# Kernel tuning notes

Measured on AMD Instinct MI355X. Metric: run time of the kernel, lower is better.

The kernel has to match this reference:

```python
import jax, jax.numpy as jnp
import numpy as np

B, S, DIM = 2, 2048, 1024
N_HEAD, HEAD_DIM = 16, 64


def setup_inputs() -> dict:
    key = jax.random.key(0)
    k1, k2, k3, k4 = jax.random.split(key, 4)
    x = jax.random.normal(k1, (B, S, DIM), dtype=jnp.float32)
    # rotary table: cos/sin pairs, shape [S, head_dim//2, 2]
    half = HEAD_DIM // 2
    inv_freq = 1.0 / (10000.0 ** (jnp.arange(0, half, dtype=jnp.float32) / half))
    t = jnp.arange(S, dtype=jnp.float32)
    ang = t[:, None] * inv_freq[None, :]
    freqs_cis = jnp.stack([jnp.cos(ang), jnp.sin(ang)], axis=-1)  # [S, half, 2]
    # causal boolean mask [1,1,S,S] (True = attend)
    mask = jnp.tril(jnp.ones((S, S), dtype=bool))[None, None]
    wqkv = jax.random.normal(k2, (3 * DIM, DIM), dtype=jnp.float32) * (DIM ** -0.5)
    wo = jax.random.normal(k3, (DIM, DIM), dtype=jnp.float32) * (DIM ** -0.5)
    return {"x": x, "freqs_cis": freqs_cis, "mask": mask, "wqkv": wqkv, "wo": wo}


def apply_rotary_emb(x, freqs_cis):
    # x: [B, S, H, D]; freqs_cis: [S, D//2, 2]
    xs = x.reshape(*x.shape[:-1], -1, 2)  # [B,S,H,D//2,2]
    fc = freqs_cis[None, :, None, :, :]  # [1,S,1,D//2,2]
    xr, xi = xs[..., 0], xs[..., 1]
    cr, ci = fc[..., 0], fc[..., 1]
    out = jnp.stack([xr * cr - xi * ci, xi * cr + xr * ci], axis=-1)
    return out.reshape(x.shape)


def reference(x, freqs_cis, mask, wqkv, wo):
    bsz, seqlen, _ = x.shape
    qkv = jnp.einsum('bsd,ed->bse', x, wqkv)  # [B,S,3*dim]
    q, k, v = jnp.split(qkv, 3, axis=-1)
    q = q.reshape(bsz, seqlen, N_HEAD, HEAD_DIM)
    k = k.reshape(bsz, seqlen, N_HEAD, HEAD_DIM)
    v = v.reshape(bsz, seqlen, N_HEAD, HEAD_DIM)
    q = apply_rotary_emb(q, freqs_cis)
    k = apply_rotary_emb(k, freqs_cis)
    scale = HEAD_DIM ** -0.5
    scores = jnp.einsum('bqhd,bkhd->bhqk', q, k) * scale  # [B,H,S,S]
    scores = jnp.where(mask, scores, jnp.finfo(scores.dtype).min)
    attn = jax.nn.softmax(scores, axis=-1)
    y = jnp.einsum('bhqk,bkhd->bqhd', attn, v).reshape(bsz, seqlen, N_HEAD * HEAD_DIM)
    return jnp.einsum('bse,de->bsd', y, wo)
```

## Files before the change

kernel.cpp:

```cpp
#include <hip/hip_runtime.h>
#include <hip/hip_bf16.h>
#include <stdint.h>


typedef __attribute__((ext_vector_type(8))) __bf16 bf16x8;
typedef __attribute__((ext_vector_type(4))) float f32x4;

union B8 { uint4 u; bf16x8 v; unsigned short us[8]; };

static __device__ __forceinline__ float bf2f(unsigned short u) {
  union { unsigned int ui; float f; } x; x.ui = ((unsigned int)u) << 16; return x.f;
}
static __device__ __forceinline__ unsigned short f2bf(float f) {
  union { float f; unsigned int ui; } x; x.f = f;
  unsigned int r = x.ui + 0x7fffu + ((x.ui >> 16) & 1u);
  return (unsigned short)(r >> 16);
}
static __device__ __forceinline__ f32x4 mfma16(bf16x8 a, bf16x8 b, f32x4 c) {
  return __builtin_amdgcn_mfma_f32_16x16x32_bf16(a, b, c, 0, 0, 0);
}
#define AS1 __attribute__((address_space(1)))
#define AS3 __attribute__((address_space(3)))
static __device__ __forceinline__ void gload_lds16(const void* g, void* l) {
  __builtin_amdgcn_global_load_lds((const AS1 unsigned int*)g,
                                   (AS3 unsigned int*)l, 16, 0, 0);
}

__global__ __launch_bounds__(256) void cvt_all_kernel(
    const float* __restrict__ x, const float* __restrict__ wqkv,
    const float* __restrict__ wo,
    unsigned short* __restrict__ xb, unsigned short* __restrict__ wqkvb,
    unsigned short* __restrict__ wob) {
  int i = blockIdx.x * 256 + threadIdx.x;
  const float* src; unsigned short* dst; int off;
  if (i < 1048576)       { src = x;    dst = xb;    off = i; }
  else if (i < 1835008)  { src = wqkv; dst = wqkvb; off = i - 1048576; }
  else                   { src = wo;   dst = wob;   off = i - 1835008; }
  float4 f = ((const float4*)src)[off];
  ushort4 u;
  u.x = f2bf(f.x); u.y = f2bf(f.y); u.z = f2bf(f.z); u.w = f2bf(f.w);
  ((ushort4*)dst)[off] = u;
}

__global__ __launch_bounds__(256) void qkv_rope_kernel(
    const unsigned short* __restrict__ xb,
    const unsigned short* __restrict__ wqkvb,
    const float* __restrict__ freqs,
    unsigned short* __restrict__ Q,
    unsigned short* __restrict__ K,
    unsigned short* __restrict__ Vt)
{
  __shared__ __align__(16) unsigned short As[128 * 64];
  __shared__ __align__(16) unsigned short Bs[128 * 64];
  const int t = threadIdx.x;
  const int lane = t & 63, wv = t >> 6;
  const int c = lane & 15, quad = lane >> 4;
  const int wm = wv >> 1, wn = wv & 1;
  const int tm = blockIdx.x & 31, tn = blockIdx.x >> 5;
  const int m0 = tm * 128, n0 = tn * 128;

  f32x4 acc[4][4] = {};

  for (int k0 = 0; k0 < 1024; k0 += 64) {
    for (int r = 0; r < 4; ++r) {
      int cid = t + 256 * r;
      int row = cid >> 3, jc = cid & 7;
      int sc = jc ^ (row & 7);
      gload_lds16(xb    + (size_t)(m0 + row) * 1024 + k0 + sc * 8, (char*)As + cid * 16);
      gload_lds16(wqkvb + (size_t)(n0 + row) * 1024 + k0 + sc * 8, (char*)Bs + cid * 16);
    }
    __syncthreads();
    for (int ks = 0; ks < 2; ++ks) {
      bf16x8 a[4], b[4];
      for (int st = 0; st < 4; ++st) {
        int ra = wm * 64 + st * 16 + c;
        int sa = (ks * 4 + quad) ^ (ra & 7);
        a[st] = *(const bf16x8*)((const char*)As + ra * 128 + sa * 16);
        int rb = wn * 64 + st * 16 + c;
        int sb = (ks * 4 + quad) ^ (rb & 7);
        b[st] = *(const bf16x8*)((const char*)Bs + rb * 128 + sb * 16);
      }
      for (int sm = 0; sm < 4; ++sm)
        for (int sn = 0; sn < 4; ++sn)
          acc[sm][sn] = mfma16(a[sm], b[sn], acc[sm][sn]);
    }
    __syncthreads();
  }

  for (int sm = 0; sm < 4; ++sm) {
    for (int sn = 0; sn < 4; ++sn) {
      const int e = n0 + wn * 64 + sn * 16 + c;
      const int seg = e >> 10;
      const int eh = e & 1023;
      const int h = eh >> 6, d = eh & 63;
      for (int i = 0; i < 4; ++i) {
        const int m = m0 + wm * 64 + sm * 16 + quad * 4 + i;
        const int b_ = m >> 11, s_ = m & 2047;
        float v = acc[sm][sn][i];
        if (seg == 2) {
          Vt[((size_t)(b_ * 16 + h) * 64 + d) * 2048 + s_] = f2bf(v);
        } else {
          float partner = __shfl_xor(v, 1, 64);
          const int p = d >> 1;
          float cr = freqs[s_ * 64 + p * 2];
          float ci = freqs[s_ * 64 + p * 2 + 1];
          float outv = (d & 1) ? (v * cr + partner * ci) : (v * cr - partner * ci);
          unsigned short* dst = (seg == 0) ? Q : K;
          dst[((size_t)(b_ * 16 + h) * 2048 + s_) * 64 + d] = f2bf(outv);
        }
      }
    }
  }
}

struct QState {
  bf16x8 qf0, qf1;
  f32x4 o[4];
  float lp[4];
};

static __device__ __forceinline__ void attn_chunk(
    QState& st, const char* Ks, const char* Vs, float* myp,
    int c, int quad, int k0, int q0, bool diag)
{
  f32x4 sfr[4];
  for (int kc = 0; kc < 4; ++kc) {
    const int key = kc * 16 + c;
    const int s0 = quad ^ (key & 7), s1 = (4 + quad) ^ (key & 7);
    f32x4 sacc = {};
    sacc = mfma16(st.qf0, *(const bf16x8*)(Ks + key * 128 + s0 * 16), sacc);
    sacc = mfma16(st.qf1, *(const bf16x8*)(Ks + key * 128 + s1 * 16), sacc);
    sfr[kc] = sacc;
  }
  for (int i = 0; i < 4; ++i) {
    const int qrow = q0 + quad * 4 + i;
    float e[4];
    for (int kc = 0; kc < 4; ++kc) {
      float arg = fmaf(sfr[kc][i], 0.18033688f, -20.19773057f);
      if (diag && (k0 + kc * 16 + c > qrow)) arg = -1e30f;
      e[kc] = exp2f(arg);
    }
    st.lp[i] += (e[0] + e[1]) + (e[2] + e[3]);
    const int prow = (quad * 4 + i) * 68;
    myp[prow + c]      = e[0];
    myp[prow + 16 + c] = e[1];
    myp[prow + 32 + c] = e[2];
    myp[prow + 48 + c] = e[3];
  }
  bf16x8 pf[2];
  for (int sH = 0; sH < 2; ++sH) {
    const float* src = myp + c * 68 + sH * 32 + quad * 8;
    float4 f0 = *(const float4*)(src);
    float4 f1 = *(const float4*)(src + 4);
    B8 p;
    p.us[0] = f2bf(f0.x); p.us[1] = f2bf(f0.y);
    p.us[2] = f2bf(f0.z); p.us[3] = f2bf(f0.w);
    p.us[4] = f2bf(f1.x); p.us[5] = f2bf(f1.y);
    p.us[6] = f2bf(f1.z); p.us[7] = f2bf(f1.w);
    pf[sH] = p.v;
  }
  for (int ct = 0; ct < 4; ++ct) {
    const int d = ct * 16 + c;
    const int s0 = quad ^ (d & 7), s1 = (4 + quad) ^ (d & 7);
    st.o[ct] = mfma16(pf[0], *(const bf16x8*)(Vs + d * 128 + s0 * 16), st.o[ct]);
    st.o[ct] = mfma16(pf[1], *(const bf16x8*)(Vs + d * 128 + s1 * 16), st.o[ct]);
  }
}

__global__ __launch_bounds__(256) void attn_partial_kernel(
    const unsigned short* __restrict__ Q,
    const unsigned short* __restrict__ K,
    const unsigned short* __restrict__ Vt,
    unsigned short* __restrict__ Po,
    float* __restrict__ Pl)
{
  __shared__ __align__(16) unsigned short Ks[64 * 64];
  __shared__ __align__(16) unsigned short Vs[64 * 64];
  __shared__ __align__(16) float plds[4][16 * 68];
  const int t = threadIdx.x;
  const int lane = t & 63, wv = t >> 6;
  const int c = lane & 15, quad = lane >> 4;
  const int bh = blockIdx.x & 31;
  const int rest = blockIdx.x >> 5;
  const int j = rest >> 1, half = rest & 1;
  const int qA = j * 64 + wv * 16;
  const int qB = (31 - j) * 64 + wv * 16;

  const unsigned short* Qb = Q + (size_t)bh * (2048 * 64);
  const unsigned short* Kb = K + (size_t)bh * (2048 * 64);
  const unsigned short* Vb = Vt + (size_t)bh * (64 * 2048);

  QState A = {}, Bst = {};
  A.qf0 = *(const bf16x8*)(Qb + (qA + c) * 64 + quad * 8);
  A.qf1 = *(const bf16x8*)(Qb + (qA + c) * 64 + 32 + quad * 8);
  Bst.qf0 = *(const bf16x8*)(Qb + (qB + c) * 64 + quad * 8);
  Bst.qf1 = *(const bf16x8*)(Qb + (qB + c) * 64 + 32 + quad * 8);

  float* myp = plds[wv];
  const int ktmax = 31 - j;

  for (int kt = half; kt <= ktmax; kt += 2) {
    const int k0 = kt * 64;
    __syncthreads();
    for (int r = 0; r < 2; ++r) {
      int cid = t + 256 * r;
      int row = cid >> 3, jc = cid & 7;
      int sc = jc ^ (row & 7);
      gload_lds16(Kb + (size_t)(k0 + row) * 64 + sc * 8, (char*)Ks + cid * 16);
      gload_lds16(Vb + (size_t)row * 2048 + k0 + sc * 8, (char*)Vs + cid * 16);
    }
    __syncthreads();
    attn_chunk(Bst, (const char*)Ks, (const char*)Vs, myp, c, quad,
               k0, qB, kt == ktmax);
    if (kt <= j)
      attn_chunk(A, (const char*)Ks, (const char*)Vs, myp, c, quad,
                 k0, qA, kt == j);
  }

  unsigned short* Poh = Po + (size_t)half * (32 * 2048 * 64) + (size_t)bh * (2048 * 64);
  float* Plh = Pl + (size_t)half * (32 * 2048) + bh * 2048;
  for (int set = 0; set < 2; ++set) {
    QState& st = set ? Bst : A;
    const int q0 = set ? qB : qA;
    for (int i = 0; i < 4; ++i) {
      float l = st.lp[i];
      l += __shfl_xor(l, 1, 16);
      l += __shfl_xor(l, 2, 16);
      l += __shfl_xor(l, 4, 16);
      l += __shfl_xor(l, 8, 16);
      const int s = q0 + quad * 4 + i;
      for (int ct = 0; ct < 4; ++ct)
        Poh[(size_t)s * 64 + ct * 16 + c] = f2bf(st.o[ct][i]);
      if (c == 0) Plh[s] = l;
    }
  }
}

__global__ __launch_bounds__(256) void combine_kernel(
    const unsigned short* __restrict__ Po, const float* __restrict__ Pl,
    unsigned short* __restrict__ Yb)
{
  const int idx = blockIdx.x * 256 + threadIdx.x;
  const int bh = idx >> 14, rem = idx & 16383;
  const int s = rem >> 3, g = rem & 7;
  const size_t base = (size_t)bh * (2048 * 64) + (size_t)s * 64 + g * 8;
  B8 a, b;
  a.u = *(const uint4*)(Po + base);
  b.u = *(const uint4*)(Po + (size_t)(32 * 2048 * 64) + base);
  float l = Pl[bh * 2048 + s] + Pl[32 * 2048 + bh * 2048 + s];
  float inv = 1.0f / l;
  B8 y;
  for (int k = 0; k < 8; ++k)
    y.us[k] = f2bf((bf2f(a.us[k]) + bf2f(b.us[k])) * inv);
  const int b_ = bh >> 4, h = bh & 15;
  *(uint4*)(Yb + ((size_t)(b_ * 2048 + s)) * 1024 + h * 64 + g * 8) = y.u;
}

__global__ __launch_bounds__(256) void attn_kernel(
    const unsigned short* __restrict__ Q,
    const unsigned short* __restrict__ K,
    const unsigned short* __restrict__ Vt,
    unsigned short* __restrict__ Y)
{
  __shared__ __align__(16) unsigned short Ks[64 * 64];
  __shared__ __align__(16) unsigned short Vs[64 * 64];
  __shared__ __align__(16) float plds[4][16 * 68];
  const int t = threadIdx.x;
  const int lane = t & 63, wv = t >> 6;
  const int c = lane & 15, quad = lane >> 4;
  const int j = blockIdx.x >> 5, bh = blockIdx.x & 31;
  const int b = bh >> 4, h = bh & 15;
  const int qA = j * 64 + wv * 16;
  const int qB = (31 - j) * 64 + wv * 16;

  const unsigned short* Qb = Q + (size_t)bh * (2048 * 64);
  const unsigned short* Kb = K + (size_t)bh * (2048 * 64);
  const unsigned short* Vb = Vt + (size_t)bh * (64 * 2048);

  QState A = {}, Bst = {};
  A.qf0 = *(const bf16x8*)(Qb + (qA + c) * 64 + quad * 8);
  A.qf1 = *(const bf16x8*)(Qb + (qA + c) * 64 + 32 + quad * 8);
  Bst.qf0 = *(const bf16x8*)(Qb + (qB + c) * 64 + quad * 8);
  Bst.qf1 = *(const bf16x8*)(Qb + (qB + c) * 64 + 32 + quad * 8);

  const int nkt = 32 - j;
  float* myp = plds[wv];

  for (int kt = 0; kt < nkt; ++kt) {
    const int k0 = kt * 64;
    __syncthreads();
    for (int r = 0; r < 2; ++r) {
      int cid = t + 256 * r;
      int row = cid >> 3, jc = cid & 7;
      int sc = jc ^ (row & 7);
      gload_lds16(Kb + (size_t)(k0 + row) * 64 + sc * 8, (char*)Ks + cid * 16);
      gload_lds16(Vb + (size_t)row * 2048 + k0 + sc * 8, (char*)Vs + cid * 16);
    }
    __syncthreads();
    attn_chunk(Bst, (const char*)Ks, (const char*)Vs, myp, c, quad,
               k0, qB, kt == 31 - j);
    if (kt <= j)
      attn_chunk(A, (const char*)Ks, (const char*)Vs, myp, c, quad,
                 k0, qA, kt == j);
  }

  for (int set = 0; set < 2; ++set) {
    QState& st = set ? Bst : A;
    const int q0 = set ? qB : qA;
    for (int i = 0; i < 4; ++i) {
      float l = st.lp[i];
      l += __shfl_xor(l, 1, 16);
      l += __shfl_xor(l, 2, 16);
      l += __shfl_xor(l, 4, 16);
      l += __shfl_xor(l, 8, 16);
      float inv = 1.0f / l;
      const int s = q0 + quad * 4 + i;
      unsigned short* dst = Y + ((size_t)(b * 2048 + s)) * 1024 + h * 64;
      for (int ct = 0; ct < 4; ++ct)
        dst[ct * 16 + c] = f2bf(st.o[ct][i] * inv);
    }
  }
}

__global__ __launch_bounds__(256) void out_proj_kernel(
    const unsigned short* __restrict__ Y,
    const unsigned short* __restrict__ wob,
    float* __restrict__ out)
{
  __shared__ __align__(16) unsigned short As[64 * 64];
  __shared__ __align__(16) unsigned short Bs[64 * 64];
  const int t = threadIdx.x;
  const int lane = t & 63, wv = t >> 6;
  const int c = lane & 15, quad = lane >> 4;
  const int wm = wv >> 1, wn = wv & 1;
  const int tm = blockIdx.x & 63, tn = blockIdx.x >> 6;
  const int m0 = tm * 64, n0 = tn * 64;

  f32x4 acc[2][2] = {};

  for (int k0 = 0; k0 < 1024; k0 += 64) {
    for (int r = 0; r < 2; ++r) {
      int cid = t + 256 * r;
      int row = cid >> 3, jc = cid & 7;
      int sc = jc ^ (row & 7);
      gload_lds16(Y   + (size_t)(m0 + row) * 1024 + k0 + sc * 8, (char*)As + cid * 16);
      gload_lds16(wob + (size_t)(n0 + row) * 1024 + k0 + sc * 8, (char*)Bs + cid * 16);
    }
    __syncthreads();
    for (int ks = 0; ks < 2; ++ks) {
      bf16x8 a[2], b[2];
      for (int st = 0; st < 2; ++st) {
        int ra = wm * 32 + st * 16 + c;
        int sa = (ks * 4 + quad) ^ (ra & 7);
        a[st] = *(const bf16x8*)((const char*)As + ra * 128 + sa * 16);
        int rb = wn * 32 + st * 16 + c;
        int sb = (ks * 4 + quad) ^ (rb & 7);
        b[st] = *(const bf16x8*)((const char*)Bs + rb * 128 + sb * 16);
      }
      for (int sm = 0; sm < 2; ++sm)
        for (int sn = 0; sn < 2; ++sn)
          acc[sm][sn] = mfma16(a[sm], b[sn], acc[sm][sn]);
    }
    __syncthreads();
  }

  for (int sm = 0; sm < 2; ++sm)
    for (int sn = 0; sn < 2; ++sn)
      for (int i = 0; i < 4; ++i) {
        const int m = m0 + wm * 32 + sm * 16 + quad * 4 + i;
        const int e = n0 + wn * 32 + sn * 16 + c;
        out[(size_t)m * 1024 + e] = acc[sm][sn][i];
      }
}

extern "C" void kernel_launch(void* const* d_in, const int* in_sizes, int n_in,
                              void* d_out, int out_size, void* d_ws, size_t ws_size,
                              hipStream_t stream) {
  const float* x     = (const float*)d_in[0];
  const float* freqs = (const float*)d_in[1];
  const float* wqkv  = (const float*)d_in[3];
  const float* wo    = (const float*)d_in[4];
  float* out = (float*)d_out;

  const size_t BHSD = (size_t)2 * 16 * 2048 * 64;
  unsigned short* Q     = (unsigned short*)d_ws;
  unsigned short* K     = Q + BHSD;
  unsigned short* Vt    = K + BHSD;
  unsigned short* Yb    = Vt + BHSD;
  unsigned short* xb    = Yb + BHSD;
  unsigned short* wqkvb = xb + 4194304;
  unsigned short* wob   = wqkvb + 3145728;
  unsigned short* Po    = wob + 1048576;
  float*          Pl    = (float*)(Po + 2 * BHSD);

  const size_t need_fast =
      (size_t)((char*)(Pl + 2 * 32 * 2048) - (char*)d_ws);

  cvt_all_kernel<<<8192, 256, 0, stream>>>(x, wqkv, wo, xb, wqkvb, wob);
  qkv_rope_kernel<<<768, 256, 0, stream>>>(xb, wqkvb, freqs, Q, K, Vt);
  if (ws_size >= need_fast) {
    attn_partial_kernel<<<1024, 256, 0, stream>>>(Q, K, Vt, Po, Pl);
    combine_kernel<<<2048, 256, 0, stream>>>(Po, Pl, Yb);
  } else {
    attn_kernel<<<512, 256, 0, stream>>>(Q, K, Vt, Yb);
  }
  out_proj_kernel<<<1024, 256, 0, stream>>>(Yb, wob, out);
}
```

Before: 229.0 us.

## Use 32x32x16 MFMA in QKV GEMM and stage bf16 probabilities in LDS

The QKV projection GEMM switches from 16x16x32 MFMA tiles to 32x32x16 MFMA, with a 2x2 grid of 16-wide accumulators per wave, and remaps the epilogue row/column indexing to match. The aim is fewer LDS fragment loads and MFMA issues per unit of work. The attention kernels now convert softmax probabilities to bf16 before writing them to LDS and read them back directly as bf16x8 fragments, which halves the LDS scratch size and removes the per-element conversion after the read. The rotary epilogue indexing is simplified, and the Q fragment loads are factored into a helper.

```diff
diff --git a/kernel.cpp b/kernel.cpp
--- a/kernel.cpp
+++ b/kernel.cpp
@@ -5,6 +5,7 @@
 
 typedef __attribute__((ext_vector_type(8))) __bf16 bf16x8;
 typedef __attribute__((ext_vector_type(4))) float f32x4;
+typedef __attribute__((ext_vector_type(16))) float f32x16;
 
 union B8 { uint4 u; bf16x8 v; unsigned short us[8]; };
 
@@ -18,6 +19,9 @@
 }
 static __device__ __forceinline__ f32x4 mfma16(bf16x8 a, bf16x8 b, f32x4 c) {
   return __builtin_amdgcn_mfma_f32_16x16x32_bf16(a, b, c, 0, 0, 0);
+}
+static __device__ __forceinline__ f32x16 mfma32(bf16x8 a, bf16x8 b, f32x16 c) {
+  return __builtin_amdgcn_mfma_f32_32x32x16_bf16(a, b, c, 0, 0, 0);
 }
 #define AS1 __attribute__((address_space(1)))
 #define AS3 __attribute__((address_space(3)))
@@ -54,12 +58,12 @@
   __shared__ __align__(16) unsigned short Bs[128 * 64];
   const int t = threadIdx.x;
   const int lane = t & 63, wv = t >> 6;
-  const int c = lane & 15, quad = lane >> 4;
+  const int l31 = lane & 31, lh = lane >> 5;
   const int wm = wv >> 1, wn = wv & 1;
   const int tm = blockIdx.x & 31, tn = blockIdx.x >> 5;
   const int m0 = tm * 128, n0 = tn * 128;
 
-  f32x4 acc[4][4] = {};
+  f32x16 acc[2][2] = {};
 
   for (int k0 = 0; k0 < 1024; k0 += 64) {
     for (int r = 0; r < 4; ++r) {
@@ -70,40 +74,38 @@
       gload_lds16(wqkvb + (size_t)(n0 + row) * 1024 + k0 + sc * 8, (char*)Bs + cid * 16);
     }
     __syncthreads();
-    for (int ks = 0; ks < 2; ++ks) {
-      bf16x8 a[4], b[4];
-      for (int st = 0; st < 4; ++st) {
-        int ra = wm * 64 + st * 16 + c;
-        int sa = (ks * 4 + quad) ^ (ra & 7);
-        a[st] = *(const bf16x8*)((const char*)As + ra * 128 + sa * 16);
-        int rb = wn * 64 + st * 16 + c;
-        int sb = (ks * 4 + quad) ^ (rb & 7);
-        b[st] = *(const bf16x8*)((const char*)Bs + rb * 128 + sb * 16);
+    for (int kst = 0; kst < 4; ++kst) {
+      const int g = kst * 2 + lh;
+      bf16x8 a[2], b[2];
+      for (int s2 = 0; s2 < 2; ++s2) {
+        int ra = wm * 64 + s2 * 32 + l31;
+        a[s2] = *(const bf16x8*)((const char*)As + ra * 128 + (g ^ (ra & 7)) * 16);
+        int rb = wn * 64 + s2 * 32 + l31;
+        b[s2] = *(const bf16x8*)((const char*)Bs + rb * 128 + (g ^ (rb & 7)) * 16);
       }
-      for (int sm = 0; sm < 4; ++sm)
-        for (int sn = 0; sn < 4; ++sn)
-          acc[sm][sn] = mfma16(a[sm], b[sn], acc[sm][sn]);
-    }
-    __syncthreads();
-  }
-
-  for (int sm = 0; sm < 4; ++sm) {
-    for (int sn = 0; sn < 4; ++sn) {
-      const int e = n0 + wn * 64 + sn * 16 + c;
+      for (int sm = 0; sm < 2; ++sm)
+        for (int sn = 0; sn < 2; ++sn)
+          acc[sm][sn] = mfma32(a[sm], b[sn], acc[sm][sn]);
+    }
+    __syncthreads();
+  }
+
+  for (int sm = 0; sm < 2; ++sm) {
+    for (int sn = 0; sn < 2; ++sn) {
+      const int e = n0 + wn * 64 + sn * 32 + l31;
       const int seg = e >> 10;
       const int eh = e & 1023;
       const int h = eh >> 6, d = eh & 63;
-      for (int i = 0; i < 4; ++i) {
-        const int m = m0 + wm * 64 + sm * 16 + quad * 4 + i;
+      for (int r = 0; r < 16; ++r) {
+        const int m = m0 + wm * 64 + sm * 32 + (r & 3) + 8 * (r >> 2) + 4 * lh;
         const int b_ = m >> 11, s_ = m & 2047;
-        float v = acc[sm][sn][i];
+        float v = acc[sm][sn][r];
         if (seg == 2) {
           Vt[((size_t)(b_ * 16 + h) * 64 + d) * 2048 + s_] = f2bf(v);
         } else {
           float partner = __shfl_xor(v, 1, 64);
-          const int p = d >> 1;
-          float cr = freqs[s_ * 64 + p * 2];
-          float ci = freqs[s_ * 64 + p * 2 + 1];
+          float cr = freqs[s_ * 64 + (d & ~1)];
+          float ci = freqs[s_ * 64 + (d | 1)];
           float outv = (d & 1) ? (v * cr + partner * ci) : (v * cr - partner * ci);
           unsigned short* dst = (seg == 0) ? Q : K;
           dst[((size_t)(b_ * 16 + h) * 2048 + s_) * 64 + d] = f2bf(outv);
@@ -119,8 +121,14 @@
   float lp[4];
 };
 
+static __device__ __forceinline__ void load_q(QState& st,
+    const unsigned short* Qb, int q0, int c, int quad) {
+  st.qf0 = *(const bf16x8*)(Qb + (q0 + c) * 64 + quad * 8);
+  st.qf1 = *(const bf16x8*)(Qb + (q0 + c) * 64 + 32 + quad * 8);
+}
+
 static __device__ __forceinline__ void attn_chunk(
-    QState& st, const char* Ks, const char* Vs, float* myp,
+    QState& st, const char* Ks, const char* Vs, unsigned short* myp,
     int c, int quad, int k0, int q0, bool diag)
 {
   f32x4 sfr[4];
@@ -141,24 +149,15 @@
       e[kc] = exp2f(arg);
     }
     st.lp[i] += (e[0] + e[1]) + (e[2] + e[3]);
-    const int prow = (quad * 4 + i) * 68;
-    myp[prow + c]      = e[0];
-    myp[prow + 16 + c] = e[1];
-    myp[prow + 32 + c] = e[2];
-    myp[prow + 48 + c] = e[3];
+    unsigned short* prow = myp + (quad * 4 + i) * 72;
+    prow[c]      = f2bf(e[0]);
+    prow[16 + c] = f2bf(e[1]);
+    prow[32 + c] = f2bf(e[2]);
+    prow[48 + c] = f2bf(e[3]);
   }
   bf16x8 pf[2];
-  for (int sH = 0; sH < 2; ++sH) {
-    const float* src = myp + c * 68 + sH * 32 + quad * 8;
-    float4 f0 = *(const float4*)(src);
-    float4 f1 = *(const float4*)(src + 4);
-    B8 p;
-    p.us[0] = f2bf(f0.x); p.us[1] = f2bf(f0.y);
-    p.us[2] = f2bf(f0.z); p.us[3] = f2bf(f0.w);
-    p.us[4] = f2bf(f1.x); p.us[5] = f2bf(f1.y);
-    p.us[6] = f2bf(f1.z); p.us[7] = f2bf(f1.w);
-    pf[sH] = p.v;
-  }
+  pf[0] = *(const bf16x8*)(myp + c * 72 + quad * 8);
+  pf[1] = *(const bf16x8*)(myp + c * 72 + 32 + quad * 8);
   for (int ct = 0; ct < 4; ++ct) {
     const int d = ct * 16 + c;
     const int s0 = quad ^ (d & 7), s1 = (4 + quad) ^ (d & 7);
@@ -176,7 +175,7 @@
 {
   __shared__ __align__(16) unsigned short Ks[64 * 64];
   __shared__ __align__(16) unsigned short Vs[64 * 64];
-  __shared__ __align__(16) float plds[4][16 * 68];
+  __shared__ __align__(16) unsigned short plds[4][16 * 72];
   const int t = threadIdx.x;
   const int lane = t & 63, wv = t >> 6;
   const int c = lane & 15, quad = lane >> 4;
@@ -191,12 +190,10 @@
   const unsigned short* Vb = Vt + (size_t)bh * (64 * 2048);
 
   QState A = {}, Bst = {};
-  A.qf0 = *(const bf16x8*)(Qb + (qA + c) * 64 + quad * 8);
-  A.qf1 = *(const bf16x8*)(Qb + (qA + c) * 64 + 32 + quad * 8);
-  Bst.qf0 = *(const bf16x8*)(Qb + (qB + c) * 64 + quad * 8);
-  Bst.qf1 = *(const bf16x8*)(Qb + (qB + c) * 64 + 32 + quad * 8);
-
-  float* myp = plds[wv];
+  load_q(A, Qb, qA, c, quad);
+  load_q(Bst, Qb, qB, c, quad);
+
+  unsigned short* myp = plds[wv];
   const int ktmax = 31 - j;
 
   for (int kt = half; kt <= ktmax; kt += 2) {
@@ -264,7 +261,7 @@
 {
   __shared__ __align__(16) unsigned short Ks[64 * 64];
   __shared__ __align__(16) unsigned short Vs[64 * 64];
-  __shared__ __align__(16) float plds[4][16 * 68];
+  __shared__ __align__(16) unsigned short plds[4][16 * 72];
   const int t = threadIdx.x;
   const int lane = t & 63, wv = t >> 6;
   const int c = lane & 15, quad = lane >> 4;
@@ -278,13 +275,11 @@
   const unsigned short* Vb = Vt + (size_t)bh * (64 * 2048);
 
   QState A = {}, Bst = {};
-  A.qf0 = *(const bf16x8*)(Qb + (qA + c) * 64 + quad * 8);
-  A.qf1 = *(const bf16x8*)(Qb + (qA + c) * 64 + 32 + quad * 8);
-  Bst.qf0 = *(const bf16x8*)(Qb + (qB + c) * 64 + quad * 8);
-  Bst.qf1 = *(const bf16x8*)(Qb + (qB + c) * 64 + 32 + quad * 8);
+  load_q(A, Qb, qA, c, quad);
+  load_q(Bst, Qb, qB, c, quad);
 
   const int nkt = 32 - j;
-  float* myp = plds[wv];
+  unsigned short* myp = plds[wv];
 
   for (int kt = 0; kt < nkt; ++kt) {
     const int k0 = kt * 64;
```

After: 221.0 us. 1.04x faster.
